# Kernel tuning notes

Measured on AMD Instinct MI355X. Metric: run time of the kernel, lower is better.

## Reference

```python
import jax, jax.numpy as jnp
import numpy as np

N_MET = 100_000
N_RXN = 50_000
E_SUB = 2_000_000
E_ALL = 4_000_000
MSG_DIM = 16
HIDDEN = 32


def setup_inputs() -> dict:
    key = jax.random.key(0)
    ks = jax.random.split(key, 16)
    x_met = jax.random.normal(ks[0], (N_MET,), dtype=jnp.float32)
    sto_sub = jax.random.uniform(ks[1], (E_SUB,), dtype=jnp.float32, minval=0.0, maxval=1.0)
    sto_all = jax.random.normal(ks[2], (E_ALL,), dtype=jnp.float32)
    met_sub = jax.random.randint(ks[3], (E_SUB,), 0, N_MET)
    rxn_sub = jax.random.randint(ks[4], (E_SUB,), 0, N_RXN)
    met_all = jax.random.randint(ks[5], (E_ALL,), 0, N_MET)
    rxn_all = jax.random.randint(ks[6], (E_ALL,), 0, N_RXN)
    # msg_mlp: Linear(2->HIDDEN), Tanh, Linear(HIDDEN->MSG_DIM)
    W1m = jax.random.normal(ks[7], (2, HIDDEN), jnp.float32) / np.sqrt(2.0)
    b1m = jnp.zeros((HIDDEN,), jnp.float32)
    W2m = jax.random.normal(ks[8], (HIDDEN, MSG_DIM), jnp.float32) / np.sqrt(HIDDEN)
    b2m = jnp.zeros((MSG_DIM,), jnp.float32)
    # rate_mlp: Linear(MSG_DIM->HIDDEN), Tanh, Linear(HIDDEN->1)
    W1r = jax.random.normal(ks[9], (MSG_DIM, HIDDEN), jnp.float32) / np.sqrt(MSG_DIM)
    b1r = jnp.zeros((HIDDEN,), jnp.float32)
    W2r = jax.random.normal(ks[10], (HIDDEN, 1), jnp.float32) / np.sqrt(HIDDEN)
    b2r = jnp.zeros((1,), jnp.float32)
    return {
        "x_met": x_met, "sto_sub": sto_sub, "sto_all": sto_all,
        "W1m": W1m, "b1m": b1m, "W2m": W2m, "b2m": b2m,
        "W1r": W1r, "b1r": b1r, "W2r": W2r, "b2r": b2r,
        "met_sub": met_sub, "rxn_sub": rxn_sub,
        "met_all": met_all, "rxn_all": rxn_all,
    }


def reference(x_met, sto_sub, sto_all, W1m, b1m, W2m, b2m, W1r, b1r, W2r, b2r,
              met_sub, rxn_sub, met_all, rxn_all):
    # gather substrate node features and build per-edge MLP input [E_sub, 2]
    msg_in = jnp.stack([x_met[met_sub], sto_sub], axis=-1)
    # msg MLP: tanh hidden, linear out -> [E_sub, MSG_DIM]
    msg = jnp.tanh(msg_in @ W1m + b1m) @ W2m + b2m
    # scatter-add messages into reactions -> [N_RXN, MSG_DIM]
    h_rxn = jax.ops.segment_sum(msg, rxn_sub, num_segments=N_RXN)
    # rate MLP + softplus -> per-reaction rate v [N_RXN]
    v = jax.nn.softplus((jnp.tanh(h_rxn @ W1r + b1r) @ W2r + b2r)[:, 0])
    # stoichiometric contributions scattered into metabolites -> dxdt [N_MET]
    contrib = sto_all * v[rxn_all]
    dxdt = jax.ops.segment_sum(contrib, met_all, num_segments=N_MET)
    return dxdt, v
```

## Files before the change

kernel.cpp:

```cpp
#include <hip/hip_runtime.h>

#define N_MET 100000
#define N_RXN 50000
#define E_SUB 2000000
#define E_ALL 4000000
#define MSG_DIM 16
#define HIDDEN 32

#define NBKT_A 391
#define NB_ALL 245
#define TILE_A 16384
#define NBKT_S 782
#define NB_SUB 245
#define TILE_S 8192


__device__ __forceinline__ float fast_tanh(float x) {
    const float ax = fabsf(x);
    const float e = __expf(2.0f * ax);
    const float t = 1.0f - 2.0f * __builtin_amdgcn_rcpf(e + 1.0f);
    return copysignf(t, x);
}


__global__ __launch_bounds__(1024) void hist_pair_kernel(
    const int* __restrict__ rxn_sub, const int* __restrict__ met_all,
    int* __restrict__ histS, int* __restrict__ histA)
{
    __shared__ int hb[NBKT_S];
    const int t = threadIdx.x, bk = blockIdx.x;
    if (bk < NB_SUB) {
        for (int i = t; i < NBKT_S; i += 1024) hb[i] = 0;
        __syncthreads();
#pragma unroll
        for (int k = 0; k < 2; ++k) {
            const int i = bk * 2048 + (k << 10) + t;
            if (i < E_SUB / 4) {
                const int4 r = ((const int4*)rxn_sub)[i];
                atomicAdd(&hb[r.x >> 6], 1);
                atomicAdd(&hb[r.y >> 6], 1);
                atomicAdd(&hb[r.z >> 6], 1);
                atomicAdd(&hb[r.w >> 6], 1);
            }
        }
        __syncthreads();
        for (int i = t; i < NBKT_S; i += 1024) histS[bk * NBKT_S + i] = hb[i];
    } else {
        const int ba = bk - NB_SUB;
        for (int i = t; i < NBKT_A; i += 1024) hb[i] = 0;
        __syncthreads();
#pragma unroll
        for (int k = 0; k < 4; ++k) {
            const int i = ba * 4096 + (k << 10) + t;
            if (i < E_ALL / 4) {
                const int4 m = ((const int4*)met_all)[i];
                atomicAdd(&hb[m.x >> 8], 1);
                atomicAdd(&hb[m.y >> 8], 1);
                atomicAdd(&hb[m.z >> 8], 1);
                atomicAdd(&hb[m.w >> 8], 1);
            }
        }
        __syncthreads();
        for (int i = t; i < NBKT_A; i += 1024) histA[ba * NBKT_A + i] = hb[i];
    }
}


__global__ __launch_bounds__(256) void scan_cols_pair_kernel(
    int* __restrict__ histS, int* __restrict__ histA,
    int* __restrict__ tot_s, int* __restrict__ tot_a)
{
    __shared__ int wsum[4];
    int* hist; int* tot; int nbkt, b;
    if ((int)blockIdx.x < NBKT_S) {
        hist = histS; tot = tot_s; nbkt = NBKT_S; b = blockIdx.x;
    } else {
        hist = histA; tot = tot_a; nbkt = NBKT_A; b = blockIdx.x - NBKT_S;
    }
    const int t = threadIdx.x, lane = t & 63, w = t >> 6;
    const int val = (t < 245) ? hist[(size_t)t * nbkt + b] : 0;
    int x = val;
#pragma unroll
    for (int off = 1; off < 64; off <<= 1) {
        const int y = __shfl_up(x, off);
        if (lane >= off) x += y;
    }
    if (lane == 63) wsum[w] = x;
    __syncthreads();
    if (w == 0) {
        int s = (lane < 4) ? wsum[lane] : 0;
#pragma unroll
        for (int off = 1; off < 4; off <<= 1) {
            const int y = __shfl_up(s, off);
            if (lane >= off) s += y;
        }
        if (lane < 4) wsum[lane] = s;
    }
    __syncthreads();
    const int excl = ((w > 0) ? wsum[w - 1] : 0) + x - val;
    if (t < 245) hist[(size_t)t * nbkt + b] = excl;
    if (t == 0) tot[b] = wsum[3];
}

__global__ __launch_bounds__(256) void scan_base_pair_kernel(
    const int* __restrict__ tot_s, int* __restrict__ base_s,
    const int* __restrict__ tot_a, int* __restrict__ base_a)
{
    __shared__ int wsum[4];
    const int* tot; int* base; int nbkt;
    if (blockIdx.x == 0) { tot = tot_s; base = base_s; nbkt = NBKT_S; }
    else                 { tot = tot_a; base = base_a; nbkt = NBKT_A; }
    const int t = threadIdx.x, lane = t & 63, w = t >> 6;
    int carry = 0;
    for (int basei = 0; basei < nbkt; basei += 256) {
        const int i = basei + t;
        const int val = (i < nbkt) ? tot[i] : 0;
        int x = val;
#pragma unroll
        for (int off = 1; off < 64; off <<= 1) {
            const int y = __shfl_up(x, off);
            if (lane >= off) x += y;
        }
        if (lane == 63) wsum[w] = x;
        __syncthreads();
        if (w == 0) {
            int s = (lane < 4) ? wsum[lane] : 0;
#pragma unroll
            for (int off = 1; off < 4; off <<= 1) {
                const int y = __shfl_up(s, off);
                if (lane >= off) s += y;
            }
            if (lane < 4) wsum[lane] = s;
        }
        __syncthreads();
        const int excl = carry + ((w > 0) ? wsum[w - 1] : 0) + x - val;
        if (i < nbkt) base[i] = excl;
        carry += wsum[3];
        __syncthreads();
    }
}


__global__ __launch_bounds__(1024) void scatter_bin_sub_kernel(
    const float* __restrict__ x_met, const float* __restrict__ sto_sub,
    const int* __restrict__ met_sub, const int* __restrict__ rxn_sub,
    const int* __restrict__ hist, const int* __restrict__ base,
    float2* __restrict__ pxs)
{
    __shared__ float2 se[TILE_S];
    __shared__ int cnt[NBKT_S];
    __shared__ int loff[NBKT_S + 1];
    __shared__ int goff[NBKT_S];
    const int t = threadIdx.x, bk = blockIdx.x;
    for (int i = t; i < NBKT_S; i += 1024) {
        cnt[i] = 0;
        goff[i] = hist[bk * NBKT_S + i] + base[i];
    }
    __syncthreads();

    const int e0 = bk * TILE_S;
    const int rem = min(TILE_S, E_SUB - e0);
    const int tb = 8 * t;
    float2 pay[8]; int meta[8];
    if (tb + 8 <= rem) {
        const int4 r01 = ((const int4*)(rxn_sub + e0))[2 * t];
        const int4 r23 = ((const int4*)(rxn_sub + e0))[2 * t + 1];
        const int4 m01 = ((const int4*)(met_sub + e0))[2 * t];
        const int4 m23 = ((const int4*)(met_sub + e0))[2 * t + 1];
        const float4 s01 = ((const float4*)(sto_sub + e0))[2 * t];
        const float4 s23 = ((const float4*)(sto_sub + e0))[2 * t + 1];
        const int rr[8] = {r01.x, r01.y, r01.z, r01.w, r23.x, r23.y, r23.z, r23.w};
        const int mm[8] = {m01.x, m01.y, m01.z, m01.w, m23.x, m23.y, m23.z, m23.w};
        const float ss[8] = {s01.x, s01.y, s01.z, s01.w, s23.x, s23.y, s23.z, s23.w};
#pragma unroll
        for (int k = 0; k < 8; ++k) {
            const int r = rr[k];
            const float x = x_met[mm[k]];
            const int sb = (__float_as_int(ss[k]) & ~63) | (r & 63);
            pay[k] = make_float2(x, __int_as_float(sb));
            const int q = r >> 6;
            meta[k] = (atomicAdd(&cnt[q], 1) << 10) | q;
        }
    } else {
#pragma unroll
        for (int k = 0; k < 8; ++k) {
            const int e = e0 + tb + k;
            if (e < E_SUB) {
                const int r = rxn_sub[e];
                const float x = x_met[met_sub[e]];
                const int sb = (__float_as_int(sto_sub[e]) & ~63) | (r & 63);
                pay[k] = make_float2(x, __int_as_float(sb));
                const int q = r >> 6;
                meta[k] = (atomicAdd(&cnt[q], 1) << 10) | q;
            } else meta[k] = -1;
        }
    }
    __syncthreads();

    if (t < 64) {
        int carry = 0;
        for (int bb = 0; bb < NBKT_S; bb += 64) {
            const int idx = bb + t;
            const int val = (idx < NBKT_S) ? cnt[idx] : 0;
            int x = val;
#pragma unroll
            for (int off = 1; off < 64; off <<= 1) {
                const int y = __shfl_up(x, off);
                if (t >= off) x += y;
            }
            if (idx < NBKT_S) loff[idx] = carry + x - val;
            carry += __shfl(x, 63);
        }
        if (t == 0) loff[NBKT_S] = carry;
    }
    __syncthreads();

#pragma unroll
    for (int k = 0; k < 8; ++k) {
        if (meta[k] >= 0)
            se[loff[meta[k] & 1023] + (meta[k] >> 10)] = pay[k];
    }
    __syncthreads();

    const int w = t >> 6, lane = t & 63;
    for (int q = w; q < NBKT_S; q += 16) {
        const int s = loff[q], lenq = loff[q + 1] - s, d = goff[q];
        for (int i = lane; i < lenq; i += 64)
            pxs[d + i] = se[s + i];
    }
}

__global__ __launch_bounds__(512, 6) void bucket_msg_kernel(
    const float2* __restrict__ pxs,
    const int* __restrict__ base, const int* __restrict__ tot,
    const float* __restrict__ W1m, const float* __restrict__ b1m,
    const float* __restrict__ W2m, const float* __restrict__ b2m,
    const float* __restrict__ W1r, const float* __restrict__ b1r,
    const float* __restrict__ W2r, const float* __restrict__ b2r,
    float* __restrict__ v)
{
    __shared__ float2 se[4096];
    __shared__ float  sth[64 * 33];
    __shared__ int    cnt[64];
    __shared__ int    soff[65];
    __shared__ int    ccnt[64];
    __shared__ float  sW2m[HIDDEN * MSG_DIM];
    __shared__ float  sb2m[MSG_DIM];
    __shared__ float  sW1r[MSG_DIM * HIDDEN];
    __shared__ float  sb1r[HIDDEN];
    __shared__ float  sW2r[HIDDEN];
    __shared__ float  sb2r;
    __shared__ float  sh[64 * 17];

    const int t = threadIdx.x;
    const int w = t >> 6, l = t & 63;
    const int half = l >> 5, j = l & 31;

    for (int i = t; i < HIDDEN * MSG_DIM; i += 512) sW2m[i] = W2m[i];
    for (int i = t; i < MSG_DIM * HIDDEN; i += 512) sW1r[i] = W1r[i];
    if (t < MSG_DIM) sb2m[t] = b2m[t];
    if (t < HIDDEN) sb1r[t] = b1r[t];
    if (t >= 64 && t < 64 + HIDDEN) sW2r[t - 64] = W2r[t - 64];
    if (t == 128) sb2r = b2r[0];
    if (t < 64) ccnt[t] = 0;

    const float w1x = W1m[j];
    const float w1y = W1m[HIDDEN + j];
    const float w1b = b1m[j];

    const int b = blockIdx.x;
    const int beg = base[b];
    const int end = beg + tot[b];

    float acc[4] = {0.0f, 0.0f, 0.0f, 0.0f};

    for (int cb = beg; cb < end; cb += 4096) {
        if (t < 64) cnt[t] = 0;
        __syncthreads();

        float2 pay[8];
        int meta[8];
#pragma unroll
        for (int k = 0; k < 8; ++k) {
            const int idx = cb + t + (k << 9);
            if (idx < end) {
                const float2 pv = pxs[idx];
                const int r = __float_as_int(pv.y) & 63;
                meta[k] = (atomicAdd(&cnt[r], 1) << 6) | r;
                pay[k] = pv;
            } else meta[k] = -1;
        }
        __syncthreads();

        if (t < 64) {
            const int orig = cnt[t];
            int x = orig;
#pragma unroll
            for (int off = 1; off < 64; off <<= 1) {
                const int y = __shfl_up(x, off);
                if (t >= off) x += y;
            }
            soff[t] = x - orig;
            if (t == 63) soff[64] = x;
            ccnt[t] += orig;
        }
        __syncthreads();

#pragma unroll
        for (int k = 0; k < 8; ++k) {
            if (meta[k] >= 0)
                se[soff[meta[k] & 63] + (meta[k] >> 6)] = pay[k];
        }
        __syncthreads();

#pragma unroll
        for (int p = 0; p < 4; ++p) {
            const int q = (w << 3) + (p << 1) + half;
            const int rb = soff[q];
            const int rl = soff[q + 1] - rb;
            float a0 = 0.0f, a1 = 0.0f;
            int i = 0;
            for (; i + 2 <= rl; i += 2) {
                const float2 e0 = se[rb + i];
                const float2 e1 = se[rb + i + 1];
                a0 += fast_tanh(fmaf(e0.x, w1x, fmaf(e0.y, w1y, w1b)));
                a1 += fast_tanh(fmaf(e1.x, w1x, fmaf(e1.y, w1y, w1b)));
            }
            if (i < rl) {
                const float2 e0 = se[rb + i];
                a0 += fast_tanh(fmaf(e0.x, w1x, fmaf(e0.y, w1y, w1b)));
            }
            acc[p] += a0 + a1;
        }
        __syncthreads();
    }

#pragma unroll
    for (int p = 0; p < 4; ++p) {
        const int q = (w << 3) + (p << 1) + half;
        sth[q * 33 + j] = acc[p];
    }
    __syncthreads();

    {
        const int r = t & 63, g = (t >> 6) << 1;
        const float cntf = (float)ccnt[r];
        float h0 = cntf * sb2m[g + 0], h1 = cntf * sb2m[g + 1];
#pragma unroll 8
        for (int jj = 0; jj < HIDDEN; ++jj) {
            const float ts = sth[r * 33 + jj];
            h0 = fmaf(ts, sW2m[jj * MSG_DIM + g + 0], h0);
            h1 = fmaf(ts, sW2m[jj * MSG_DIM + g + 1], h1);
        }
        sh[r * 17 + g + 0] = h0;
        sh[r * 17 + g + 1] = h1;
    }
    __syncthreads();

    if (t < 64) {
        const int r = b * 64 + t;
        if (r < N_RXN) {
            float h[MSG_DIM];
#pragma unroll
            for (int d = 0; d < MSG_DIM; ++d) h[d] = sh[t * 17 + d];
            float acc2 = sb2r;
#pragma unroll 2
            for (int jj = 0; jj < HIDDEN; ++jj) {
                float z = sb1r[jj];
#pragma unroll
                for (int d = 0; d < MSG_DIM; ++d)
                    z = fmaf(h[d], sW1r[d * HIDDEN + jj], z);
                acc2 = fmaf(fast_tanh(z), sW2r[jj], acc2);
            }
            v[r] = fmaxf(acc2, 0.0f) + log1pf(expf(-fabsf(acc2)));
        }
    }
}


__global__ __launch_bounds__(1024) void scatter_bin_kernel(
    const float* __restrict__ sto_all, const float* __restrict__ v,
    const int* __restrict__ met_all, const int* __restrict__ rxn_all,
    const int* __restrict__ hist, const int* __restrict__ base,
    float* __restrict__ pc)
{
    __shared__ float sp[TILE_A];
    __shared__ int cnt[NBKT_A];
    __shared__ int loff[NBKT_A + 1];
    __shared__ int goff[NBKT_A];
    const int t = threadIdx.x, bk = blockIdx.x;
    for (int i = t; i < NBKT_A; i += 1024) {
        cnt[i] = 0;
        goff[i] = hist[bk * NBKT_A + i] + base[i];
    }
    __syncthreads();

    const int e0 = bk * TILE_A;
    const int rem = min(TILE_A, E_ALL - e0);
    const int tb = 16 * t;
    int meta[16];
    const bool full = (tb + 16 <= rem);
    if (full) {
#pragma unroll
        for (int kk = 0; kk < 4; ++kk) {
            const int4 m = ((const int4*)(met_all + e0))[4 * t + kk];
            meta[4 * kk + 0] = (atomicAdd(&cnt[m.x >> 8], 1) << 17) | m.x;
            meta[4 * kk + 1] = (atomicAdd(&cnt[m.y >> 8], 1) << 17) | m.y;
            meta[4 * kk + 2] = (atomicAdd(&cnt[m.z >> 8], 1) << 17) | m.z;
            meta[4 * kk + 3] = (atomicAdd(&cnt[m.w >> 8], 1) << 17) | m.w;
        }
    } else {
#pragma unroll
        for (int k = 0; k < 16; ++k) {
            const int e = e0 + tb + k;
            if (e < E_ALL) {
                const int m = met_all[e];
                meta[k] = (atomicAdd(&cnt[m >> 8], 1) << 17) | m;
            } else meta[k] = -1;
        }
    }
    __syncthreads();

    if (t < 64) {
        int carry = 0;
        for (int bb = 0; bb < NBKT_A; bb += 64) {
            const int idx = bb + t;
            const int val = (idx < NBKT_A) ? cnt[idx] : 0;
            int x = val;
#pragma unroll
            for (int off = 1; off < 64; off <<= 1) {
                const int y = __shfl_up(x, off);
                if (t >= off) x += y;
            }
            if (idx < NBKT_A) loff[idx] = carry + x - val;
            carry += __shfl(x, 63);
        }
        if (t == 0) loff[NBKT_A] = carry;
    }
    __syncthreads();

    if (full) {
#pragma unroll
        for (int kk = 0; kk < 4; ++kk) {
            const int4 r = ((const int4*)(rxn_all + e0))[4 * t + kk];
            const float4 s = ((const float4*)(sto_all + e0))[4 * t + kk];
            const int rr[4] = {r.x, r.y, r.z, r.w};
            const float ss[4] = {s.x, s.y, s.z, s.w};
#pragma unroll
            for (int u = 0; u < 4; ++u) {
                const int mt = meta[4 * kk + u];
                const int m = mt & 0x1FFFF;
                const float c = ss[u] * v[rr[u]];
                const int cb = (__float_as_int(c) & ~255) | (m & 255);
                sp[loff[m >> 8] + (mt >> 17)] = __int_as_float(cb);
            }
        }
    } else {
#pragma unroll
        for (int k = 0; k < 16; ++k) {
            const int e = e0 + tb + k;
            if (e < E_ALL) {
                const int mt = meta[k];
                const int m = mt & 0x1FFFF;
                const float c = sto_all[e] * v[rxn_all[e]];
                const int cb = (__float_as_int(c) & ~255) | (m & 255);
                sp[loff[m >> 8] + (mt >> 17)] = __int_as_float(cb);
            }
        }
    }
    __syncthreads();

    const int w = t >> 6, lane = t & 63;
    for (int q = w; q < NBKT_A; q += 16) {
        const int s = loff[q], lenq = loff[q + 1] - s, d = goff[q];
        for (int i = lane; i < lenq; i += 64)
            pc[d + i] = sp[s + i];
    }
}

__global__ __launch_bounds__(512) void bucket_accum_kernel(
    const float* __restrict__ pc,
    const int* __restrict__ base, const int* __restrict__ tot,
    float* __restrict__ dxdt)
{
    __shared__ float acc[256];
    const int b = blockIdx.x, t = threadIdx.x;
    if (t < 256) acc[t] = 0.0f;
    __syncthreads();
    const int beg = base[b];
    const int end = beg + tot[b];
    int a0 = (beg + 3) & ~3;
    if (a0 > end) a0 = end;
    const int a1 = a0 + ((end - a0) & ~3);
    for (int i = beg + t; i < a0; i += 512) {
        const float pv = pc[i];
        atomicAdd(&acc[__float_as_int(pv) & 255], pv);
    }
    for (int i = a0 + 4 * t; i < a1; i += 2048) {
        const float4 pv = *(const float4*)(pc + i);
        atomicAdd(&acc[__float_as_int(pv.x) & 255], pv.x);
        atomicAdd(&acc[__float_as_int(pv.y) & 255], pv.y);
        atomicAdd(&acc[__float_as_int(pv.z) & 255], pv.z);
        atomicAdd(&acc[__float_as_int(pv.w) & 255], pv.w);
    }
    for (int i = a1 + t; i < end; i += 512) {
        const float pv = pc[i];
        atomicAdd(&acc[__float_as_int(pv) & 255], pv);
    }
    __syncthreads();
    if (t < 256) {
        const int met = b * 256 + t;
        if (met < N_MET) dxdt[met] = acc[t];
    }
}

extern "C" void kernel_launch(void* const* d_in, const int* in_sizes, int n_in,
                              void* d_out, int out_size, void* d_ws, size_t ws_size,
                              hipStream_t stream) {
    const float* x_met   = (const float*)d_in[0];
    const float* sto_sub = (const float*)d_in[1];
    const float* sto_all = (const float*)d_in[2];
    const float* W1m     = (const float*)d_in[3];
    const float* b1m     = (const float*)d_in[4];
    const float* W2m     = (const float*)d_in[5];
    const float* b2m     = (const float*)d_in[6];
    const float* W1r     = (const float*)d_in[7];
    const float* b1r     = (const float*)d_in[8];
    const float* W2r     = (const float*)d_in[9];
    const float* b2r     = (const float*)d_in[10];
    const int*   met_sub = (const int*)d_in[11];
    const int*   rxn_sub = (const int*)d_in[12];
    const int*   met_all = (const int*)d_in[13];
    const int*   rxn_all = (const int*)d_in[14];

    float* dxdt = (float*)d_out;
    float* v    = dxdt + N_MET;

    char* ws = (char*)d_ws;
    int* histS  = (int*)ws;  ws += (((size_t)NB_SUB * NBKT_S * 4 + 15) / 16) * 16;
    int* histA  = (int*)ws;  ws += (((size_t)NB_ALL * NBKT_A * 4 + 15) / 16) * 16;
    int* tot_s  = (int*)ws;  ws += ((sizeof(int) * NBKT_S + 15) / 16) * 16;
    int* base_s = (int*)ws;  ws += ((sizeof(int) * NBKT_S + 15) / 16) * 16;
    int* tot_a  = (int*)ws;  ws += ((sizeof(int) * NBKT_A + 15) / 16) * 16;
    int* base_a = (int*)ws;  ws += ((sizeof(int) * NBKT_A + 15) / 16) * 16;
    char* P = ws;
    float2* pxs = (float2*)P;
    float*  pc  = (float*)P;

    hist_pair_kernel<<<NB_SUB + NB_ALL, 1024, 0, stream>>>(
        rxn_sub, met_all, histS, histA);
    scan_cols_pair_kernel<<<NBKT_S + NBKT_A, 256, 0, stream>>>(
        histS, histA, tot_s, tot_a);
    scan_base_pair_kernel<<<2, 256, 0, stream>>>(tot_s, base_s, tot_a, base_a);

    scatter_bin_sub_kernel<<<NB_SUB, 1024, 0, stream>>>(
        x_met, sto_sub, met_sub, rxn_sub, histS, base_s, pxs);
    bucket_msg_kernel<<<NBKT_S, 512, 0, stream>>>(
        pxs, base_s, tot_s, W1m, b1m, W2m, b2m, W1r, b1r, W2r, b2r, v);

    scatter_bin_kernel<<<NB_ALL, 1024, 0, stream>>>(
        sto_all, v, met_all, rxn_all, histA, base_a, pc);
    bucket_accum_kernel<<<NBKT_A, 512, 0, stream>>>(pc, base_a, tot_a, dxdt);
}
```

Baseline: 251.9 us.

## Drop global histogram for all-edge pass; write tile-local sorted segments with offsets

Removes the separate histogram and scan passes for met_all. The scatter kernel now writes each tile's locally bucket-sorted contributions contiguously with float4 stores and records per-tile bucket offsets. The accumulation kernel then walks every tile's segment for its bucket, using wave shuffles to distribute the offsets. This saves reading met_all once and drops the scattered global writes, in exchange for many short, fragmented reads per bucket in the accumulation kernel.

```diff
diff --git a/kernel.cpp b/kernel.cpp
--- a/kernel.cpp
+++ b/kernel.cpp
@@ -10,6 +10,7 @@
 #define NBKT_A 391
 #define NB_ALL 245
 #define TILE_A 16384
+#define LOFFA_W (NBKT_A + 1)
 #define NBKT_S 782
 #define NB_SUB 245
 #define TILE_S 8192
@@ -23,62 +24,35 @@
 }
 
 
-__global__ __launch_bounds__(1024) void hist_pair_kernel(
-    const int* __restrict__ rxn_sub, const int* __restrict__ met_all,
-    int* __restrict__ histS, int* __restrict__ histA)
+__global__ __launch_bounds__(1024) void hist_sub_kernel(
+    const int* __restrict__ rxn_sub, int* __restrict__ histS)
 {
     __shared__ int hb[NBKT_S];
     const int t = threadIdx.x, bk = blockIdx.x;
-    if (bk < NB_SUB) {
-        for (int i = t; i < NBKT_S; i += 1024) hb[i] = 0;
-        __syncthreads();
-#pragma unroll
-        for (int k = 0; k < 2; ++k) {
-            const int i = bk * 2048 + (k << 10) + t;
-            if (i < E_SUB / 4) {
-                const int4 r = ((const int4*)rxn_sub)[i];
-                atomicAdd(&hb[r.x >> 6], 1);
-                atomicAdd(&hb[r.y >> 6], 1);
-                atomicAdd(&hb[r.z >> 6], 1);
-                atomicAdd(&hb[r.w >> 6], 1);
-            }
-        }
-        __syncthreads();
-        for (int i = t; i < NBKT_S; i += 1024) histS[bk * NBKT_S + i] = hb[i];
-    } else {
-        const int ba = bk - NB_SUB;
-        for (int i = t; i < NBKT_A; i += 1024) hb[i] = 0;
-        __syncthreads();
-#pragma unroll
-        for (int k = 0; k < 4; ++k) {
-            const int i = ba * 4096 + (k << 10) + t;
-            if (i < E_ALL / 4) {
-                const int4 m = ((const int4*)met_all)[i];
-                atomicAdd(&hb[m.x >> 8], 1);
-                atomicAdd(&hb[m.y >> 8], 1);
-                atomicAdd(&hb[m.z >> 8], 1);
-                atomicAdd(&hb[m.w >> 8], 1);
-            }
-        }
-        __syncthreads();
-        for (int i = t; i < NBKT_A; i += 1024) histA[ba * NBKT_A + i] = hb[i];
-    }
-}
-
-
-__global__ __launch_bounds__(256) void scan_cols_pair_kernel(
-    int* __restrict__ histS, int* __restrict__ histA,
-    int* __restrict__ tot_s, int* __restrict__ tot_a)
+    for (int i = t; i < NBKT_S; i += 1024) hb[i] = 0;
+    __syncthreads();
+#pragma unroll
+    for (int k = 0; k < 2; ++k) {
+        const int i = bk * 2048 + (k << 10) + t;
+        if (i < E_SUB / 4) {
+            const int4 r = ((const int4*)rxn_sub)[i];
+            atomicAdd(&hb[r.x >> 6], 1);
+            atomicAdd(&hb[r.y >> 6], 1);
+            atomicAdd(&hb[r.z >> 6], 1);
+            atomicAdd(&hb[r.w >> 6], 1);
+        }
+    }
+    __syncthreads();
+    for (int i = t; i < NBKT_S; i += 1024) histS[bk * NBKT_S + i] = hb[i];
+}
+
+__global__ __launch_bounds__(256) void scan_cols_sub_kernel(
+    int* __restrict__ histS, int* __restrict__ tot_s)
 {
     __shared__ int wsum[4];
-    int* hist; int* tot; int nbkt, b;
-    if ((int)blockIdx.x < NBKT_S) {
-        hist = histS; tot = tot_s; nbkt = NBKT_S; b = blockIdx.x;
-    } else {
-        hist = histA; tot = tot_a; nbkt = NBKT_A; b = blockIdx.x - NBKT_S;
-    }
+    const int b = blockIdx.x;
     const int t = threadIdx.x, lane = t & 63, w = t >> 6;
-    const int val = (t < 245) ? hist[(size_t)t * nbkt + b] : 0;
+    const int val = (t < NB_SUB) ? histS[(size_t)t * NBKT_S + b] : 0;
     int x = val;
 #pragma unroll
     for (int off = 1; off < 64; off <<= 1) {
@@ -98,23 +72,19 @@
     }
     __syncthreads();
     const int excl = ((w > 0) ? wsum[w - 1] : 0) + x - val;
-    if (t < 245) hist[(size_t)t * nbkt + b] = excl;
-    if (t == 0) tot[b] = wsum[3];
-}
-
-__global__ __launch_bounds__(256) void scan_base_pair_kernel(
-    const int* __restrict__ tot_s, int* __restrict__ base_s,
-    const int* __restrict__ tot_a, int* __restrict__ base_a)
+    if (t < NB_SUB) histS[(size_t)t * NBKT_S + b] = excl;
+    if (t == 0) tot_s[b] = wsum[3];
+}
+
+__global__ __launch_bounds__(256) void scan_base_sub_kernel(
+    const int* __restrict__ tot_s, int* __restrict__ base_s)
 {
     __shared__ int wsum[4];
-    const int* tot; int* base; int nbkt;
-    if (blockIdx.x == 0) { tot = tot_s; base = base_s; nbkt = NBKT_S; }
-    else                 { tot = tot_a; base = base_a; nbkt = NBKT_A; }
     const int t = threadIdx.x, lane = t & 63, w = t >> 6;
     int carry = 0;
-    for (int basei = 0; basei < nbkt; basei += 256) {
+    for (int basei = 0; basei < NBKT_S; basei += 256) {
         const int i = basei + t;
-        const int val = (i < nbkt) ? tot[i] : 0;
+        const int val = (i < NBKT_S) ? tot_s[i] : 0;
         int x = val;
 #pragma unroll
         for (int off = 1; off < 64; off <<= 1) {
@@ -134,7 +104,7 @@
         }
         __syncthreads();
         const int excl = carry + ((w > 0) ? wsum[w - 1] : 0) + x - val;
-        if (i < nbkt) base[i] = excl;
+        if (i < NBKT_S) base_s[i] = excl;
         carry += wsum[3];
         __syncthreads();
     }
@@ -381,18 +351,13 @@
 __global__ __launch_bounds__(1024) void scatter_bin_kernel(
     const float* __restrict__ sto_all, const float* __restrict__ v,
     const int* __restrict__ met_all, const int* __restrict__ rxn_all,
-    const int* __restrict__ hist, const int* __restrict__ base,
-    float* __restrict__ pc)
+    int* __restrict__ loffA, float* __restrict__ pc)
 {
     __shared__ float sp[TILE_A];
     __shared__ int cnt[NBKT_A];
     __shared__ int loff[NBKT_A + 1];
-    __shared__ int goff[NBKT_A];
     const int t = threadIdx.x, bk = blockIdx.x;
-    for (int i = t; i < NBKT_A; i += 1024) {
-        cnt[i] = 0;
-        goff[i] = hist[bk * NBKT_A + i] + base[i];
-    }
+    for (int i = t; i < NBKT_A; i += 1024) cnt[i] = 0;
     __syncthreads();
 
     const int e0 = bk * TILE_A;
@@ -438,6 +403,8 @@
         if (t == 0) loff[NBKT_A] = carry;
     }
     __syncthreads();
+
+    if (t < LOFFA_W) loffA[bk * LOFFA_W + t] = loff[t];
 
     if (full) {
 #pragma unroll
@@ -470,46 +437,39 @@
     }
     __syncthreads();
 
+    for (int i = 4 * t; i < rem; i += 4096)
+        *(float4*)(pc + e0 + i) = *(const float4*)(sp + i);
+}
+
+__global__ __launch_bounds__(512) void bucket_accum_kernel(
+    const float* __restrict__ pc, const int* __restrict__ loffA,
+    float* __restrict__ dxdt)
+{
+    __shared__ float acc[256];
+    const int q = blockIdx.x, t = threadIdx.x;
     const int w = t >> 6, lane = t & 63;
-    for (int q = w; q < NBKT_A; q += 16) {
-        const int s = loff[q], lenq = loff[q + 1] - s, d = goff[q];
-        for (int i = lane; i < lenq; i += 64)
-            pc[d + i] = sp[s + i];
-    }
-}
-
-__global__ __launch_bounds__(512) void bucket_accum_kernel(
-    const float* __restrict__ pc,
-    const int* __restrict__ base, const int* __restrict__ tot,
-    float* __restrict__ dxdt)
-{
-    __shared__ float acc[256];
-    const int b = blockIdx.x, t = threadIdx.x;
     if (t < 256) acc[t] = 0.0f;
     __syncthreads();
-    const int beg = base[b];
-    const int end = beg + tot[b];
-    int a0 = (beg + 3) & ~3;
-    if (a0 > end) a0 = end;
-    const int a1 = a0 + ((end - a0) & ~3);
-    for (int i = beg + t; i < a0; i += 512) {
-        const float pv = pc[i];
-        atomicAdd(&acc[__float_as_int(pv) & 255], pv);
-    }
-    for (int i = a0 + 4 * t; i < a1; i += 2048) {
-        const float4 pv = *(const float4*)(pc + i);
-        atomicAdd(&acc[__float_as_int(pv.x) & 255], pv.x);
-        atomicAdd(&acc[__float_as_int(pv.y) & 255], pv.y);
-        atomicAdd(&acc[__float_as_int(pv.z) & 255], pv.z);
-        atomicAdd(&acc[__float_as_int(pv.w) & 255], pv.w);
-    }
-    for (int i = a1 + t; i < end; i += 512) {
-        const float pv = pc[i];
-        atomicAdd(&acc[__float_as_int(pv) & 255], pv);
+
+    const int nt = (NB_ALL - 1 - w) / 8 + 1;
+    int sv = 0, ev = 0;
+    if (lane < nt) {
+        const int tile = w + 8 * lane;
+        sv = loffA[tile * LOFFA_W + q];
+        ev = loffA[tile * LOFFA_W + q + 1];
+    }
+    for (int it = 0; it < nt; ++it) {
+        const int s = __shfl(sv, it);
+        const int e = __shfl(ev, it);
+        const int tbase = (w + 8 * it) * TILE_A;
+        for (int i = s + lane; i < e; i += 64) {
+            const float pv = pc[tbase + i];
+            atomicAdd(&acc[__float_as_int(pv) & 255], pv);
+        }
     }
     __syncthreads();
     if (t < 256) {
-        const int met = b * 256 + t;
+        const int met = q * 256 + t;
         if (met < N_MET) dxdt[met] = acc[t];
     }
 }
@@ -538,20 +498,16 @@
 
     char* ws = (char*)d_ws;
     int* histS  = (int*)ws;  ws += (((size_t)NB_SUB * NBKT_S * 4 + 15) / 16) * 16;
-    int* histA  = (int*)ws;  ws += (((size_t)NB_ALL * NBKT_A * 4 + 15) / 16) * 16;
     int* tot_s  = (int*)ws;  ws += ((sizeof(int) * NBKT_S + 15) / 16) * 16;
     int* base_s = (int*)ws;  ws += ((sizeof(int) * NBKT_S + 15) / 16) * 16;
-    int* tot_a  = (int*)ws;  ws += ((sizeof(int) * NBKT_A + 15) / 16) * 16;
-    int* base_a = (int*)ws;  ws += ((sizeof(int) * NBKT_A + 15) / 16) * 16;
+    int* loffA  = (int*)ws;  ws += (((size_t)NB_ALL * LOFFA_W * 4 + 15) / 16) * 16;
     char* P = ws;
     float2* pxs = (float2*)P;
     float*  pc  = (float*)P;
 
-    hist_pair_kernel<<<NB_SUB + NB_ALL, 1024, 0, stream>>>(
-        rxn_sub, met_all, histS, histA);
-    scan_cols_pair_kernel<<<NBKT_S + NBKT_A, 256, 0, stream>>>(
-        histS, histA, tot_s, tot_a);
-    scan_base_pair_kernel<<<2, 256, 0, stream>>>(tot_s, base_s, tot_a, base_a);
+    hist_sub_kernel<<<NB_SUB, 1024, 0, stream>>>(rxn_sub, histS);
+    scan_cols_sub_kernel<<<NBKT_S, 256, 0, stream>>>(histS, tot_s);
+    scan_base_sub_kernel<<<1, 256, 0, stream>>>(tot_s, base_s);
 
     scatter_bin_sub_kernel<<<NB_SUB, 1024, 0, stream>>>(
         x_met, sto_sub, met_sub, rxn_sub, histS, base_s, pxs);
@@ -559,6 +515,6 @@
         pxs, base_s, tot_s, W1m, b1m, W2m, b2m, W1r, b1r, W2r, b2r, v);
 
     scatter_bin_kernel<<<NB_ALL, 1024, 0, stream>>>(
-        sto_all, v, met_all, rxn_all, histA, base_a, pc);
-    bucket_accum_kernel<<<NBKT_A, 512, 0, stream>>>(pc, base_a, tot_a, dxdt);
-}
+        sto_all, v, met_all, rxn_all, loffA, pc);
+    bucket_accum_kernel<<<NBKT_A, 512, 0, stream>>>(pc, loffA, dxdt);
+}
```

Measured after the change: 252.3 us. About the same (+0.1%).
